# Performance work log

Measured on AMD Instinct MI355X. Metric: run time of the kernel, lower is better.

## Reference

```python
import jax, jax.numpy as jnp
import numpy as np

N_HEADS = 8
N_GROUPS = 32
EPS = 1e-5


def setup_inputs() -> dict:
    key = jax.random.key(0)
    ks = jax.random.split(key, 3)
    b, c, h, w = 8, 512, 32, 32
    x = jax.random.normal(ks[0], (b, c, h, w), dtype=jnp.float32)
    gamma = jnp.ones((c,), jnp.float32)
    beta = jnp.zeros((c,), jnp.float32)
    w_qkv = jax.random.normal(ks[1], (3 * c, c), jnp.float32) * (1.0 / np.sqrt(c))
    b_qkv = jnp.zeros((3 * c,), jnp.float32)
    w_proj = jax.random.normal(ks[2], (c, c), jnp.float32) * (1.0 / np.sqrt(c))
    b_proj = jnp.zeros((c,), jnp.float32)
    return {"x": x, "gamma": gamma, "beta": beta, "w_qkv": w_qkv,
            "b_qkv": b_qkv, "w_proj": w_proj, "b_proj": b_proj}


def _group_norm(x, gamma, beta):
    # x: [b, c, T]; GroupNorm over (c//G, T) per group, computed in fp32
    b, c, t = x.shape
    xg = x.reshape(b, N_GROUPS, c // N_GROUPS, t).astype(jnp.float32)
    mean = xg.mean(axis=(2, 3), keepdims=True)
    var = xg.var(axis=(2, 3), keepdims=True)
    xg = (xg - mean) * jax.lax.rsqrt(var + EPS)
    xn = xg.reshape(b, c, t).astype(x.dtype)
    return xn * gamma[None, :, None] + beta[None, :, None]


def reference(x, gamma, beta, w_qkv, b_qkv, w_proj, b_proj):
    b, c, *spatial = x.shape
    t = int(np.prod(spatial))
    xf = x.reshape(b, c, t)
    h = _group_norm(xf, gamma, beta)
    # 1x1 conv == channel matmul
    qkv = jnp.einsum('oc,bct->bot', w_qkv, h) + b_qkv[None, :, None]  # [b, 3c, t]
    ch = c // N_HEADS
    qkv = qkv.reshape(b * N_HEADS, 3 * ch, t)
    q, k, v = qkv[:, :ch], qkv[:, ch:2 * ch], qkv[:, 2 * ch:]
    scale = 1.0 / np.sqrt(np.sqrt(ch))
    weight = jnp.einsum('bct,bcs->bts', q * scale, k * scale)
    weight = jax.nn.softmax(weight.astype(jnp.float32), axis=-1).astype(weight.dtype)
    a = jnp.einsum('bts,bcs->bct', weight, v)  # [b*H, ch, t]
    a = a.reshape(b, c, t)
    h = jnp.einsum('oc,bct->bot', w_proj, a) + b_proj[None, :, None]
    return (xf + h).reshape(b, c, *spatial)
```

## Files before the change

### kernel.cpp

```cpp
#include <hip/hip_runtime.h>
#include <hip/hip_bf16.h>
#include <math.h>

#define BATCH 8
#define CDIM 512
#define TDIM 1024
#define NHD 8

typedef __attribute__((ext_vector_type(8))) _Float16 f16x8;
typedef __attribute__((ext_vector_type(4))) float floatx4;

#define QSCALE 0.18033688011112042f

static __device__ __forceinline__ unsigned short f2h(float f) {
    _Float16 h = (_Float16)f;
    return *reinterpret_cast<unsigned short*>(&h);
}
static __device__ __forceinline__ void async_load16(const unsigned short* gsrc,
                                                    unsigned short* ldst) {
    __builtin_amdgcn_global_load_lds(
        (const __attribute__((address_space(1))) void*)gsrc,
        (__attribute__((address_space(3))) void*)ldst, 16, 0, 0);
}

__global__ __launch_bounds__(256) void prep_kernel(
    const float* __restrict__ x, const float* __restrict__ gamma,
    const float* __restrict__ beta, const float* __restrict__ w_qkv,
    const float* __restrict__ w_proj, unsigned short* __restrict__ h_t,
    unsigned short* __restrict__ wq, unsigned short* __restrict__ wp) {
    int tid = threadIdx.x;
    if (blockIdx.x >= 256) {
        int i = (blockIdx.x - 256) * 256 + tid;
        const int nA = 1536 * 512 / 4;
        const float* s;
        unsigned short* d;
        int j;
        if (i < nA) { s = w_qkv; d = wq; j = i; }
        else        { s = w_proj; d = wp; j = i - nA; }
        float4 v = ((const float4*)s)[j];
        ushort4 o;
        o.x = f2h(v.x); o.y = f2h(v.y); o.z = f2h(v.z); o.w = f2h(v.w);
        ((ushort4*)d)[j] = o;
        return;
    }
    int bg = blockIdx.x;
    int b = bg >> 5, g = bg & 31;
    const float* xp = x + ((size_t)(b * CDIM + g * 16)) * TDIM;

    float s = 0.f, ss = 0.f;
    for (int r = 0; r < 16; ++r) {
        float4 v = ((const float4*)xp)[r * 256 + tid];
        s  += v.x + v.y + v.z + v.w;
        ss += v.x * v.x + v.y * v.y + v.z * v.z + v.w * v.w;
    }
    for (int off = 32; off > 0; off >>= 1) {
        s  += __shfl_down(s, off, 64);
        ss += __shfl_down(ss, off, 64);
    }
    __shared__ float rs[4], rss[4], stat[2];
    int wave = tid >> 6;
    if ((tid & 63) == 0) { rs[wave] = s; rss[wave] = ss; }
    __syncthreads();
    if (tid == 0) {
        float S  = rs[0] + rs[1] + rs[2] + rs[3];
        float SS = rss[0] + rss[1] + rss[2] + rss[3];
        float mean = S * (1.f / 16384.f);
        float var  = SS * (1.f / 16384.f) - mean * mean;
        stat[0] = mean;
        stat[1] = rsqrtf(var + 1e-5f);
    }
    __syncthreads();
    float mean = stat[0], rstd = stat[1];

    int cpair = tid & 7, trow = tid >> 3;
    int c0 = g * 16 + cpair * 2;
    float g0 = gamma[c0] * rstd,  g1 = gamma[c0 + 1] * rstd;
    float b0 = beta[c0] - mean * g0, b1 = beta[c0 + 1] - mean * g1;
    const float* x0 = x + ((size_t)(b * CDIM + c0)) * TDIM;
    const float* x1 = x0 + TDIM;
    unsigned int* hp = (unsigned int*)h_t + (size_t)b * TDIM * 256 + g * 8 + cpair;
    for (int p = 0; p < 32; ++p) {
        int t = p * 32 + trow;
        float v0 = x0[t] * g0 + b0;
        float v1 = x1[t] * g1 + b1;
        hp[(size_t)t * 256] = (unsigned)f2h(v0) | ((unsigned)f2h(v1) << 16);
    }
}

__global__ __launch_bounds__(256) void mfma_gemm(
    const unsigned short* __restrict__ Wb,
    const unsigned short* __restrict__ Xt,
    const float* __restrict__ bias,
    int M, int K, int mode,
    unsigned short* __restrict__ q_t,
    unsigned short* __restrict__ k_t,
    unsigned short* __restrict__ v,
    const float* __restrict__ resid,
    float* __restrict__ outp) {
    __shared__ __align__(16) unsigned short As[2 * 128 * 32];
    __shared__ __align__(16) unsigned short Bs[2 * 128 * 32];

    int tid = threadIdx.x;
    int n0 = blockIdx.x * 128, m0 = blockIdx.y * 128, bb = blockIdx.z;
    const unsigned short* Xp = Xt + (size_t)bb * TDIM * K;

    int lane = tid & 63, w = tid >> 6;
    int l15 = lane & 15, quad = lane >> 4;
    int wm = w >> 1, wn = w & 1;

    const unsigned short* aSrc[4];
    const unsigned short* bSrc[4];
    unsigned short* aDst[4];
    unsigned short* bDst[4];
#pragma unroll
    for (int c = 0; c < 4; ++c) {
        int slot = w * 256 + c * 64 + lane;
        int panel = slot >> 9, row = (slot >> 2) & 127, g4 = slot & 3;
        aSrc[c] = Wb + (size_t)(m0 + row) * K + panel * 32 + g4 * 8;
        bSrc[c] = Xp + (size_t)(n0 + row) * K + panel * 32 + g4 * 8;
        aDst[c] = &As[(w * 256 + c * 64) * 8];
        bDst[c] = &Bs[(w * 256 + c * 64) * 8];
    }

    floatx4 acc[4][4];
#pragma unroll
    for (int i = 0; i < 4; ++i)
#pragma unroll
        for (int j = 0; j < 4; ++j) acc[i][j] = (floatx4){0.f, 0.f, 0.f, 0.f};

    for (int k0 = 0; k0 < K; k0 += 64) {
#pragma unroll
        for (int c = 0; c < 4; ++c) {
            async_load16(aSrc[c] + k0, aDst[c]);
            async_load16(bSrc[c] + k0, bDst[c]);
        }
        __syncthreads();
#pragma unroll
        for (int kc = 0; kc < 2; ++kc) {
            f16x8 af[4], bfr[4];
#pragma unroll
            for (int mi = 0; mi < 4; ++mi)
                af[mi] = *(const f16x8*)&As[(kc * 128 + wm * 64 + mi * 16 + l15) * 32 + quad * 8];
#pragma unroll
            for (int ni = 0; ni < 4; ++ni)
                bfr[ni] = *(const f16x8*)&Bs[(kc * 128 + wn * 64 + ni * 16 + l15) * 32 + quad * 8];
#pragma unroll
            for (int mi = 0; mi < 4; ++mi)
#pragma unroll
                for (int ni = 0; ni < 4; ++ni)
                    acc[mi][ni] = __builtin_amdgcn_mfma_f32_16x16x32_f16(
                        af[mi], bfr[ni], acc[mi][ni], 0, 0, 0);
        }
        __syncthreads();
    }

    int b8 = bb * NHD;
#pragma unroll
    for (int mi = 0; mi < 4; ++mi) {
        int mBase = m0 + wm * 64 + mi * 16 + quad * 4;
#pragma unroll
        for (int ni = 0; ni < 4; ++ni) {
            floatx4 a = acc[mi][ni];
            int n = n0 + wn * 64 + ni * 16 + l15;
            if (mode == 0) {
                int chunk = mBase >> 6;
                int hd = chunk / 3, part = chunk % 3;
                int cB = mBase & 63;
                if (part == 0) {
                    ushort4 pk;
                    pk.x = f2h((a[0] + bias[mBase + 0]) * QSCALE);
                    pk.y = f2h((a[1] + bias[mBase + 1]) * QSCALE);
                    pk.z = f2h((a[2] + bias[mBase + 2]) * QSCALE);
                    pk.w = f2h((a[3] + bias[mBase + 3]) * QSCALE);
                    *(ushort4*)&q_t[((size_t)(b8 + hd) * TDIM + n) * 64 + cB] = pk;
                } else if (part == 1) {
                    ushort4 pk;
                    pk.x = f2h(a[0] + bias[mBase + 0]);
                    pk.y = f2h(a[1] + bias[mBase + 1]);
                    pk.z = f2h(a[2] + bias[mBase + 2]);
                    pk.w = f2h(a[3] + bias[mBase + 3]);
                    *(ushort4*)&k_t[((size_t)(b8 + hd) * TDIM + n) * 64 + cB] = pk;
                } else {
#pragma unroll
                    for (int r = 0; r < 4; ++r)
                        v[((size_t)(b8 + hd) * 64 + cB + r) * TDIM + n] =
                            f2h(a[r] + bias[mBase + r]);
                }
            } else {
                size_t base = ((size_t)bb * CDIM + mBase) * TDIM + n;
#pragma unroll
                for (int r = 0; r < 4; ++r)
                    outp[base + (size_t)r * TDIM] =
                        a[r] + bias[mBase + r] + resid[base + (size_t)r * TDIM];
            }
        }
    }
}

__global__ __launch_bounds__(256, 2) void attn_kernel(
    const unsigned short* __restrict__ q_t,
    const unsigned short* __restrict__ k_t,
    const unsigned short* __restrict__ v,
    unsigned short* __restrict__ a_t) {
    __shared__ __align__(16) unsigned short Kb[2][64 * 64];
    __shared__ __align__(16) unsigned short Vb[2][64 * 64];

    int tid = threadIdx.x;
    int bh = blockIdx.x;
    int q0 = blockIdx.y * 128;
    int lane = tid & 63, w = tid >> 6;
    int l15 = lane & 15, quad = lane >> 4;
    int l7 = l15 & 7;

    const unsigned short* Qp = q_t + (size_t)bh * TDIM * 64;
    const unsigned short* Kp = k_t + (size_t)bh * TDIM * 64;
    const unsigned short* Vp = v + (size_t)bh * 64 * TDIM;

    int kofs[2], vofs[2];
    unsigned short* kdst[2];
    unsigned short* vdst[2];
#pragma unroll
    for (int c = 0; c < 2; ++c) {
        int s_ = w * 128 + c * 64 + lane;
        int m = s_ >> 3, gs = s_ & 7, g = gs ^ (m & 7);
        int mi = m >> 4, qq = (m >> 2) & 3, rr = m & 3;
        int pm = (mi & 1) * 32 + qq * 8 + (mi >> 1) * 4 + rr;
        kofs[c] = pm * 64 + g * 8;
        vofs[c] = m * TDIM + g * 8;
        kdst[c] = &Kb[0][(w * 128 + c * 64) * 8];
        vdst[c] = &Vb[0][(w * 128 + c * 64) * 8];
    }
    const int bufstep = 64 * 64;

#pragma unroll
    for (int c = 0; c < 2; ++c) {
        async_load16(Kp + kofs[c], kdst[c]);
        async_load16(Vp + vofs[c], vdst[c]);
    }

    f16x8 qf[2][2];
#pragma unroll
    for (int f = 0; f < 2; ++f)
#pragma unroll
        for (int ch = 0; ch < 2; ++ch)
            qf[f][ch] = *(const f16x8*)(Qp + (size_t)(q0 + w * 32 + f * 16 + l15) * 64 +
                                        (ch * 4 + quad) * 8);

    floatx4 o_acc[4][2];
#pragma unroll
    for (int i = 0; i < 4; ++i)
#pragma unroll
        for (int j = 0; j < 2; ++j) o_acc[i][j] = (floatx4){0.f, 0.f, 0.f, 0.f};
    float m_run[2] = {-INFINITY, -INFINITY};
    float l_run[2] = {0.f, 0.f};

    __syncthreads();

    for (int it = 0; it < 16; ++it) {
        int cur = it & 1;
        if (it < 15) {
            int s0n = (it + 1) * 64;
#pragma unroll
            for (int c = 0; c < 2; ++c) {
                async_load16(Kp + (size_t)s0n * 64 + kofs[c], kdst[c] + (cur ^ 1) * bufstep);
                async_load16(Vp + s0n + vofs[c], vdst[c] + (cur ^ 1) * bufstep);
            }
        }
        f16x8 kf[4][2];
#pragma unroll
        for (int mi = 0; mi < 4; ++mi)
#pragma unroll
            for (int ch = 0; ch < 2; ++ch)
                kf[mi][ch] = *(const f16x8*)&Kb[cur][(mi * 16 + l15) * 64 +
                                                    ((ch * 4 + quad) ^ l7) * 8];

        floatx4 sT[2][4];
#pragma unroll
        for (int f = 0; f < 2; ++f)
#pragma unroll
            for (int mi = 0; mi < 4; ++mi) {
                floatx4 z = (floatx4){0.f, 0.f, 0.f, 0.f};
                z = __builtin_amdgcn_mfma_f32_16x16x32_f16(kf[mi][0], qf[f][0], z, 0, 0, 0);
                z = __builtin_amdgcn_mfma_f32_16x16x32_f16(kf[mi][1], qf[f][1], z, 0, 0, 0);
                sT[f][mi] = z;
            }

        f16x8 vf[4][2];
#pragma unroll
        for (int ci = 0; ci < 4; ++ci)
#pragma unroll
            for (int ch = 0; ch < 2; ++ch)
                vf[ci][ch] = *(const f16x8*)&Vb[cur][(ci * 16 + l15) * 64 +
                                                    ((ch * 4 + quad) ^ l7) * 8];

        f16x8 pf[2][2];
#pragma unroll
        for (int f = 0; f < 2; ++f) {
            float mx = sT[f][0][0];
#pragma unroll
            for (int mi = 0; mi < 4; ++mi)
#pragma unroll
                for (int r = 0; r < 4; ++r) mx = fmaxf(mx, sT[f][mi][r]);
            mx = fmaxf(mx, __shfl_xor(mx, 16));
            mx = fmaxf(mx, __shfl_xor(mx, 32));
            float mn = fmaxf(m_run[f], mx);
            float alpha = __builtin_amdgcn_exp2f(m_run[f] - mn);
            float sum = 0.f;
#pragma unroll
            for (int mi = 0; mi < 4; ++mi)
#pragma unroll
                for (int r = 0; r < 4; ++r) {
                    float p = __builtin_amdgcn_exp2f(sT[f][mi][r] - mn);
                    sT[f][mi][r] = p;
                    sum += p;
                }
            sum += __shfl_xor(sum, 16);
            sum += __shfl_xor(sum, 32);
            l_run[f] = l_run[f] * alpha + sum;
            m_run[f] = mn;
#pragma unroll
            for (int ci = 0; ci < 4; ++ci) {
                o_acc[ci][f][0] *= alpha; o_acc[ci][f][1] *= alpha;
                o_acc[ci][f][2] *= alpha; o_acc[ci][f][3] *= alpha;
            }
#pragma unroll
            for (int kb = 0; kb < 2; ++kb) {
                pf[f][kb][0] = (_Float16)sT[f][kb][0];
                pf[f][kb][1] = (_Float16)sT[f][kb][1];
                pf[f][kb][2] = (_Float16)sT[f][kb][2];
                pf[f][kb][3] = (_Float16)sT[f][kb][3];
                pf[f][kb][4] = (_Float16)sT[f][kb + 2][0];
                pf[f][kb][5] = (_Float16)sT[f][kb + 2][1];
                pf[f][kb][6] = (_Float16)sT[f][kb + 2][2];
                pf[f][kb][7] = (_Float16)sT[f][kb + 2][3];
            }
        }

#pragma unroll
        for (int ci = 0; ci < 4; ++ci)
#pragma unroll
            for (int f = 0; f < 2; ++f)
#pragma unroll
                for (int kb = 0; kb < 2; ++kb)
                    o_acc[ci][f] = __builtin_amdgcn_mfma_f32_16x16x32_f16(
                        vf[ci][kb], pf[f][kb], o_acc[ci][f], 0, 0, 0);
        __syncthreads();
    }

    int b = bh >> 3, hd = bh & 7;
#pragma unroll
    for (int f = 0; f < 2; ++f) {
        float linv = 1.f / l_run[f];
        int t = q0 + w * 32 + f * 16 + l15;
        size_t rowb = ((size_t)b * TDIM + t) * CDIM + hd * 64 + quad * 4;
#pragma unroll
        for (int ci = 0; ci < 4; ++ci) {
            ushort4 pk;
            pk.x = f2h(o_acc[ci][f][0] * linv);
            pk.y = f2h(o_acc[ci][f][1] * linv);
            pk.z = f2h(o_acc[ci][f][2] * linv);
            pk.w = f2h(o_acc[ci][f][3] * linv);
            *(ushort4*)&a_t[rowb + ci * 16] = pk;
        }
    }
}

extern "C" void kernel_launch(void* const* d_in, const int* in_sizes, int n_in,
                              void* d_out, int out_size, void* d_ws, size_t ws_size,
                              hipStream_t stream) {
    (void)in_sizes; (void)n_in; (void)out_size; (void)ws_size;
    const float* x      = (const float*)d_in[0];
    const float* gamma  = (const float*)d_in[1];
    const float* beta   = (const float*)d_in[2];
    const float* w_qkv  = (const float*)d_in[3];
    const float* b_qkv  = (const float*)d_in[4];
    const float* w_proj = (const float*)d_in[5];
    const float* b_proj = (const float*)d_in[6];
    float* out = (float*)d_out;

    unsigned short* wq  = (unsigned short*)d_ws;
    unsigned short* wp  = wq + 1536 * 512;
    unsigned short* h_t = wp + 512 * 512;
    unsigned short* q_t = h_t + (size_t)BATCH * TDIM * CDIM;
    unsigned short* k_t = q_t + (size_t)64 * TDIM * 64;
    unsigned short* vv  = k_t + (size_t)64 * TDIM * 64;
    unsigned short* a_t = vv + (size_t)64 * TDIM * 64;

    prep_kernel<<<1280, 256, 0, stream>>>(x, gamma, beta, w_qkv, w_proj, h_t, wq, wp);

    mfma_gemm<<<dim3(8, 12, BATCH), 256, 0, stream>>>(
        wq, h_t, b_qkv, 1536, 512, 0, q_t, k_t, vv, nullptr, nullptr);

    attn_kernel<<<dim3(64, 8), 256, 0, stream>>>(q_t, k_t, vv, a_t);

    mfma_gemm<<<dim3(8, 4, BATCH), 256, 0, stream>>>(
        wp, a_t, b_proj, 512, 512, 1, nullptr, nullptr, nullptr, x, out);
}
```

Measured before the change: 165.9 us.

## Load GEMM weights directly to registers, shrink proj tile and attention blocks

The GEMM now reads its weight operand straight from global memory into registers instead of staging it through LDS, and it is templated on the M tile so the output projection can use 64-row tiles and launch twice as many blocks. The attention kernel drops to 128 threads covering 64 queries per block, which doubles the grid so the GPU is better filled. Each block now fetches its K/V tiles with 4 async loads per thread instead of 2. The risks are that uncoalesced per-lane weight reads leave global latency exposed with no prefetch, and that smaller attention blocks reuse each K/V tile across fewer queries, so total K/V traffic doubles.

```diff
diff --git a/kernel.cpp b/kernel.cpp
--- a/kernel.cpp
+++ b/kernel.cpp
@@ -87,77 +87,79 @@
     }
 }
 
+template <int BM>
 __global__ __launch_bounds__(256) void mfma_gemm(
     const unsigned short* __restrict__ Wb,
     const unsigned short* __restrict__ Xt,
     const float* __restrict__ bias,
-    int M, int K, int mode,
+    int K, int mode,
     unsigned short* __restrict__ q_t,
     unsigned short* __restrict__ k_t,
     unsigned short* __restrict__ v,
     const float* __restrict__ resid,
     float* __restrict__ outp) {
-    __shared__ __align__(16) unsigned short As[2 * 128 * 32];
+    constexpr int AF = BM / 32;
     __shared__ __align__(16) unsigned short Bs[2 * 128 * 32];
 
     int tid = threadIdx.x;
-    int n0 = blockIdx.x * 128, m0 = blockIdx.y * 128, bb = blockIdx.z;
+    int n0 = blockIdx.x * 128, m0 = blockIdx.y * BM, bb = blockIdx.z;
     const unsigned short* Xp = Xt + (size_t)bb * TDIM * K;
 
     int lane = tid & 63, w = tid >> 6;
     int l15 = lane & 15, quad = lane >> 4;
     int wm = w >> 1, wn = w & 1;
 
-    const unsigned short* aSrc[4];
+    const unsigned short* aBase[AF];
+#pragma unroll
+    for (int mi = 0; mi < AF; ++mi)
+        aBase[mi] = Wb + (size_t)(m0 + wm * (BM / 2) + mi * 16 + l15) * K + quad * 8;
+
     const unsigned short* bSrc[4];
-    unsigned short* aDst[4];
     unsigned short* bDst[4];
 #pragma unroll
     for (int c = 0; c < 4; ++c) {
         int slot = w * 256 + c * 64 + lane;
         int panel = slot >> 9, row = (slot >> 2) & 127, g4 = slot & 3;
-        aSrc[c] = Wb + (size_t)(m0 + row) * K + panel * 32 + g4 * 8;
         bSrc[c] = Xp + (size_t)(n0 + row) * K + panel * 32 + g4 * 8;
-        aDst[c] = &As[(w * 256 + c * 64) * 8];
         bDst[c] = &Bs[(w * 256 + c * 64) * 8];
     }
 
-    floatx4 acc[4][4];
-#pragma unroll
-    for (int i = 0; i < 4; ++i)
+    floatx4 acc[AF][4];
+#pragma unroll
+    for (int i = 0; i < AF; ++i)
 #pragma unroll
         for (int j = 0; j < 4; ++j) acc[i][j] = (floatx4){0.f, 0.f, 0.f, 0.f};
 
     for (int k0 = 0; k0 < K; k0 += 64) {
-#pragma unroll
-        for (int c = 0; c < 4; ++c) {
-            async_load16(aSrc[c] + k0, aDst[c]);
-            async_load16(bSrc[c] + k0, bDst[c]);
+        f16x8 af[AF][2];
+#pragma unroll
+        for (int mi = 0; mi < AF; ++mi)
+#pragma unroll
+            for (int kc = 0; kc < 2; ++kc)
+                af[mi][kc] = *(const f16x8*)(aBase[mi] + k0 + kc * 32);
+#pragma unroll
+        for (int c = 0; c < 4; ++c) async_load16(bSrc[c] + k0, bDst[c]);
+        __syncthreads();
+#pragma unroll
+        for (int kc = 0; kc < 2; ++kc) {
+            f16x8 bfr[4];
+#pragma unroll
+            for (int ni = 0; ni < 4; ++ni)
+                bfr[ni] = *(const f16x8*)&Bs[(kc * 128 + wn * 64 + ni * 16 + l15) * 32 + quad * 8];
+#pragma unroll
+            for (int mi = 0; mi < AF; ++mi)
+#pragma unroll
+                for (int ni = 0; ni < 4; ++ni)
+                    acc[mi][ni] = __builtin_amdgcn_mfma_f32_16x16x32_f16(
+                        af[mi][kc], bfr[ni], acc[mi][ni], 0, 0, 0);
         }
         __syncthreads();
-#pragma unroll
-        for (int kc = 0; kc < 2; ++kc) {
-            f16x8 af[4], bfr[4];
-#pragma unroll
-            for (int mi = 0; mi < 4; ++mi)
-                af[mi] = *(const f16x8*)&As[(kc * 128 + wm * 64 + mi * 16 + l15) * 32 + quad * 8];
-#pragma unroll
-            for (int ni = 0; ni < 4; ++ni)
-                bfr[ni] = *(const f16x8*)&Bs[(kc * 128 + wn * 64 + ni * 16 + l15) * 32 + quad * 8];
-#pragma unroll
-            for (int mi = 0; mi < 4; ++mi)
-#pragma unroll
-                for (int ni = 0; ni < 4; ++ni)
-                    acc[mi][ni] = __builtin_amdgcn_mfma_f32_16x16x32_f16(
-                        af[mi], bfr[ni], acc[mi][ni], 0, 0, 0);
-        }
-        __syncthreads();
     }
 
     int b8 = bb * NHD;
 #pragma unroll
-    for (int mi = 0; mi < 4; ++mi) {
-        int mBase = m0 + wm * 64 + mi * 16 + quad * 4;
+    for (int mi = 0; mi < AF; ++mi) {
+        int mBase = m0 + wm * (BM / 2) + mi * 16 + quad * 4;
 #pragma unroll
         for (int ni = 0; ni < 4; ++ni) {
             floatx4 a = acc[mi][ni];
@@ -197,7 +199,7 @@
     }
 }
 
-__global__ __launch_bounds__(256, 2) void attn_kernel(
+__global__ __launch_bounds__(128, 2) void attn_kernel(
     const unsigned short* __restrict__ q_t,
     const unsigned short* __restrict__ k_t,
     const unsigned short* __restrict__ v,
@@ -207,7 +209,7 @@
 
     int tid = threadIdx.x;
     int bh = blockIdx.x;
-    int q0 = blockIdx.y * 128;
+    int q0 = blockIdx.y * 64;
     int lane = tid & 63, w = tid >> 6;
     int l15 = lane & 15, quad = lane >> 4;
     int l7 = l15 & 7;
@@ -216,24 +218,24 @@
     const unsigned short* Kp = k_t + (size_t)bh * TDIM * 64;
     const unsigned short* Vp = v + (size_t)bh * 64 * TDIM;
 
-    int kofs[2], vofs[2];
-    unsigned short* kdst[2];
-    unsigned short* vdst[2];
-#pragma unroll
-    for (int c = 0; c < 2; ++c) {
-        int s_ = w * 128 + c * 64 + lane;
+    int kofs[4], vofs[4];
+    unsigned short* kdst[4];
+    unsigned short* vdst[4];
+#pragma unroll
+    for (int c = 0; c < 4; ++c) {
+        int s_ = w * 256 + c * 64 + lane;
         int m = s_ >> 3, gs = s_ & 7, g = gs ^ (m & 7);
         int mi = m >> 4, qq = (m >> 2) & 3, rr = m & 3;
         int pm = (mi & 1) * 32 + qq * 8 + (mi >> 1) * 4 + rr;
         kofs[c] = pm * 64 + g * 8;
         vofs[c] = m * TDIM + g * 8;
-        kdst[c] = &Kb[0][(w * 128 + c * 64) * 8];
-        vdst[c] = &Vb[0][(w * 128 + c * 64) * 8];
+        kdst[c] = &Kb[0][(w * 256 + c * 64) * 8];
+        vdst[c] = &Vb[0][(w * 256 + c * 64) * 8];
     }
     const int bufstep = 64 * 64;
 
 #pragma unroll
-    for (int c = 0; c < 2; ++c) {
+    for (int c = 0; c < 4; ++c) {
         async_load16(Kp + kofs[c], kdst[c]);
         async_load16(Vp + vofs[c], vdst[c]);
     }
@@ -261,7 +263,7 @@
         if (it < 15) {
             int s0n = (it + 1) * 64;
 #pragma unroll
-            for (int c = 0; c < 2; ++c) {
+            for (int c = 0; c < 4; ++c) {
                 async_load16(Kp + (size_t)s0n * 64 + kofs[c], kdst[c] + (cur ^ 1) * bufstep);
                 async_load16(Vp + s0n + vofs[c], vdst[c] + (cur ^ 1) * bufstep);
             }
@@ -388,11 +390,11 @@
 
     prep_kernel<<<1280, 256, 0, stream>>>(x, gamma, beta, w_qkv, w_proj, h_t, wq, wp);
 
-    mfma_gemm<<<dim3(8, 12, BATCH), 256, 0, stream>>>(
-        wq, h_t, b_qkv, 1536, 512, 0, q_t, k_t, vv, nullptr, nullptr);
-
-    attn_kernel<<<dim3(64, 8), 256, 0, stream>>>(q_t, k_t, vv, a_t);
-
-    mfma_gemm<<<dim3(8, 4, BATCH), 256, 0, stream>>>(
-        wp, a_t, b_proj, 512, 512, 1, nullptr, nullptr, nullptr, x, out);
-}
+    mfma_gemm<128><<<dim3(8, 12, BATCH), 256, 0, stream>>>(
+        wq, h_t, b_qkv, 512, 0, q_t, k_t, vv, nullptr, nullptr);
+
+    attn_kernel<<<dim3(64, 16), 128, 0, stream>>>(q_t, k_t, vv, a_t);
+
+    mfma_gemm<64><<<dim3(8, 8, BATCH), 256, 0, stream>>>(
+        wp, a_t, b_proj, 512, 1, nullptr, nullptr, nullptr, x, out);
+}
```

Result: slower. 177.5 us (+7.0%).
